# Kernel optimization log

Measured on AMD Instinct MI355X. Metric: run time of the kernel, lower is better.

Reference implementation:

```python
import jax, jax.numpy as jnp
import numpy as np

EPS = 1e-5
K = 20

def lrelu(x):
    return jnp.where(x >= 0, x, 0.2 * x)

def in2d(x):  # [B,C,N,k] instance norm over (N,k), no affine, biased var
    m = jnp.mean(x, axis=(2, 3), keepdims=True)
    v = jnp.var(x, axis=(2, 3), keepdims=True)
    return (x - m) * jax.lax.rsqrt(v + EPS)

def in1d(x):  # [B,C,N] instance norm over N
    m = jnp.mean(x, axis=2, keepdims=True)
    v = jnp.var(x, axis=2, keepdims=True)
    return (x - m) * jax.lax.rsqrt(v + EPS)

def knn_idx(x, k):  # x: [B,C,N]; uses only first 3 channels (as original)
    p = x[:, :3, :]
    inner = -2.0 * jnp.einsum('bcn,bcm->bnm', p, p)
    xx = jnp.sum(p * p, axis=1)  # [B,N]
    pd = -xx[:, :, None] - inner - xx[:, None, :]  # negative squared dist [B,N,N]
    return jax.lax.top_k(pd, k)[1]  # [B,N,k]

def graph_feature(x, k):  # x: [B,C,N] -> [B,2C,N,k]
    idx = knn_idx(x, k)
    xT = jnp.transpose(x, (0, 2, 1))  # [B,N,C]
    feat = jax.vmap(lambda t, i: t[i])(xT, idx)  # [B,N,k,C]
    center = xT[:, :, None, :]
    out = jnp.concatenate([feat - center, jnp.broadcast_to(center, feat.shape)], axis=3)
    return jnp.transpose(out, (0, 3, 1, 2))  # [B,2C,N,k]

def conv2d1(w, x):  # 1x1 conv2d: w [O,C], x [B,C,N,k]
    return jnp.einsum('oc,bcnk->bonk', w, x)

def conv1d1(w, x):  # 1x1 conv1d: w [O,C], x [B,C,N]
    return jnp.einsum('oc,bcn->bon', w, x)

def setup_inputs() -> dict:
    key = jax.random.key(0)
    ks = jax.random.split(key, 10)
    def w(k, o, c):
        return jax.random.normal(k, (o, c), dtype=jnp.float32) * np.float32(1.0 / np.sqrt(c))
    return {
        'x':  jax.random.normal(ks[0], (4, 4096, 4), dtype=jnp.float32),
        'w1': w(ks[1], 64, 8),
        'w2': w(ks[2], 64, 64),
        'w3': w(ks[3], 64, 128),
        'w4': w(ks[4], 64, 64),
        'w5': w(ks[5], 64, 128),
        'w6': w(ks[6], 1024, 192),
        'w7': w(ks[7], 512, 1216),
        'w8': w(ks[8], 256, 512),
        'w9': w(ks[9], 2, 256),
    }

def reference(x, w1, w2, w3, w4, w5, w6, w7, w8, w9):
    xt = jnp.transpose(x, (0, 2, 1))  # [B,4,N]
    num_points = xt.shape[2]
    # EdgeConv block 1
    f = graph_feature(xt, K)                     # [B,8,N,k]
    h = lrelu(in2d(conv2d1(w1, f)))
    h = lrelu(in2d(conv2d1(w2, h)))
    x1 = jnp.max(h, axis=-1)                     # [B,64,N]
    # EdgeConv block 2
    f = graph_feature(x1, K)                     # [B,128,N,k]
    h = lrelu(in2d(conv2d1(w3, f)))
    h = lrelu(in2d(conv2d1(w4, h)))
    x2 = jnp.max(h, axis=-1)
    # EdgeConv block 3
    f = graph_feature(x2, K)
    h = lrelu(in2d(conv2d1(w5, f)))
    x3 = jnp.max(h, axis=-1)
    # global embedding
    cat = jnp.concatenate([x1, x2, x3], axis=1)  # [B,192,N]
    g = lrelu(in1d(conv1d1(w6, cat)))            # [B,1024,N]
    g = jnp.max(g, axis=-1, keepdims=True)       # [B,1024,1]
    g = jnp.broadcast_to(g, (g.shape[0], g.shape[1], num_points))
    h = jnp.concatenate([g, x1, x2, x3], axis=1) # [B,1216,N]
    h = lrelu(in1d(conv1d1(w7, h)))
    h = lrelu(in1d(conv1d1(w8, h)))
    # dropout identity (eval mode)
    out = conv1d1(w9, h)                         # [B,2,N]
    return jnp.transpose(out, (0, 2, 1))         # [B,N,2]
```

## Files before the change

kernel.cpp:

```cpp
#include <hip/hip_runtime.h>
#include <math.h>

constexpr int BB  = 4;
constexpr int NN  = 4096;
constexpr int KK  = 20;
constexpr int NKK = NN * KK;
constexpr int TPOS = BB * NKK;
constexpr int NMASK = NN - 1;

#define DEVFN __device__ __forceinline__

DEVFN float lrelu_f(float v) { return v >= 0.f ? v : 0.2f * v; }
DEVFN unsigned fenc(float f) { unsigned u = __float_as_uint(f); return (u & 0x80000000u) ? ~u : (u | 0x80000000u); }
DEVFN float fdec(unsigned k) { unsigned u = (k & 0x80000000u) ? (k & 0x7fffffffu) : ~k; return __uint_as_float(u); }

template<int CSTRIDE>
__global__ __launch_bounds__(256) void knn_kernel(const float* __restrict__ xin, int* __restrict__ idxout)
{
    __shared__ float sx[NN], sy[NN], sz[NN];
    __shared__ unsigned sdist[NN];
    __shared__ unsigned shist[256];
    __shared__ unsigned scollv[256];
    __shared__ unsigned long long scoll64[128];
    __shared__ unsigned sres[2];
    __shared__ unsigned scnt[2];
    const int tid = threadIdx.x;
    const int b  = blockIdx.x >> 8;
    const int q0 = (blockIdx.x & 255) * 16;
    for (int i = tid; i < NN; i += 256) {
        const float4 rc = *reinterpret_cast<const float4*>(xin + (size_t)(b*NN + i) * CSTRIDE);
        sx[i] = rc.x; sy[i] = rc.y; sz[i] = rc.z;
    }

    for (int qq = 0; qq < 16; ++qq) {
        __syncthreads();
        shist[tid] = 0;
        if (tid == 0) { scnt[0] = 0; scnt[1] = 0; }
        const int qi = q0 + qq;
        const float qx = sx[qi], qy = sy[qi], qz = sz[qi];
        const float nxx = -__fadd_rn(__fadd_rn(__fmul_rn(qx,qx), __fmul_rn(qy,qy)), __fmul_rn(qz,qz));
        __syncthreads();
#pragma unroll
        for (int i = 0; i < NN/256; ++i) {
            const int m = tid + (i << 8);
            float cx = sx[m], cy = sy[m], cz = sz[m];
            float cw  = __fadd_rn(__fadd_rn(__fmul_rn(cx,cx), __fmul_rn(cy,cy)), __fmul_rn(cz,cz));
            float dot = __fadd_rn(__fadd_rn(__fmul_rn(qx,cx), __fmul_rn(qy,cy)), __fmul_rn(qz,cz));
            float pd  = __fsub_rn(__fsub_rn(nxx, __fmul_rn(-2.f, dot)), cw);
            unsigned u = fenc(pd);
            sdist[m] = u;
            atomicAdd(&shist[u >> 24], 1u);
        }
        __syncthreads();
        if (tid < 64) {
            const int base = 255 - tid*4;
            unsigned h0 = shist[base], h1 = shist[base-1], h2 = shist[base-2], h3 = shist[base-3];
            unsigned s = h0 + h1 + h2 + h3;
            unsigned c = s;
#pragma unroll
            for (int off = 1; off < 64; off <<= 1) { unsigned t = __shfl_up(c, off, 64); if (tid >= off) c += t; }
            unsigned cprev = c - s;
            if (c >= KK && cprev < KK) {
                unsigned cc = cprev; int bb = base;
                if (cc + h0 < KK) { cc += h0; bb = base-1;
                    if (cc + h1 < KK) { cc += h1; bb = base-2;
                        if (cc + h2 < KK) { cc += h2; bb = base-3; } } }
                sres[0] = (unsigned)bb; sres[1] = KK - cc;
            }
        }
        __syncthreads();
        const unsigned b0 = sres[0], K1 = sres[1];
        shist[tid] = 0;
        __syncthreads();
#pragma unroll
        for (int i = 0; i < NN/256; ++i) {
            unsigned u = sdist[tid + (i << 8)];
            if ((u >> 24) == b0) atomicAdd(&shist[(u >> 16) & 255u], 1u);
        }
        __syncthreads();
        if (tid < 64) {
            const int base = 255 - tid*4;
            unsigned h0 = shist[base], h1 = shist[base-1], h2 = shist[base-2], h3 = shist[base-3];
            unsigned s = h0 + h1 + h2 + h3;
            unsigned c = s;
#pragma unroll
            for (int off = 1; off < 64; off <<= 1) { unsigned t = __shfl_up(c, off, 64); if (tid >= off) c += t; }
            unsigned cprev = c - s;
            if (c >= K1 && cprev < K1) {
                unsigned cc = cprev; int bb = base;
                if (cc + h0 < K1) { cc += h0; bb = base-1;
                    if (cc + h1 < K1) { cc += h1; bb = base-2;
                        if (cc + h2 < K1) { cc += h2; bb = base-3; } } }
                sres[0] = (unsigned)bb; sres[1] = K1 - cc;
            }
        }
        __syncthreads();
        const unsigned prefix16 = (b0 << 8) | sres[0];
        const unsigned K2 = sres[1];
#pragma unroll
        for (int i = 0; i < NN/256; ++i) {
            unsigned u = sdist[tid + (i << 8)];
            if ((u >> 16) == prefix16) {
                unsigned pos = atomicAdd(&scnt[0], 1u);
                if (pos < 256u) scollv[pos] = u;
            }
        }
        __syncthreads();
        {
            int cb = (int)scnt[0]; if (cb > 256) cb = 256;
            if (tid < cb) {
                unsigned v = scollv[tid];
                unsigned ng = 0, ne = 0;
                for (int j = 0; j < cb; ++j) {
                    unsigned w = scollv[j];
                    ng += (w > v); ne += (w == v);
                }
                if (ng < K2 && ng + ne >= K2) sres[0] = v;
            }
        }
        __syncthreads();
        const unsigned W = sres[0];
#pragma unroll
        for (int i = 0; i < NN/256; ++i) {
            const int m = tid + (i << 8);
            unsigned u = sdist[m];
            if (u >= W) {
                unsigned pos = atomicAdd(&scnt[1], 1u);
                if (pos < 128u) scoll64[pos] = ((unsigned long long)u << 32) | (unsigned)(NN-1 - m);
            }
        }
        __syncthreads();
        {
            int c2 = (int)scnt[1]; if (c2 > 128) c2 = 128;
            if (tid < c2) {
                unsigned long long kv = scoll64[tid];
                int rank = 0;
                for (int j = 0; j < c2; ++j) rank += (scoll64[j] > kv);
                if (rank < KK) {
                    int* op = idxout + ((size_t)(b*NN + qi)) * KK;
                    op[rank] = (NN-1) - (int)(kv & 0xFFFFFFFFull);
                }
            }
        }
    }
}

template<int CINH, int CSTRIDE>
__global__ __launch_bounds__(64) void uv_kernel(const float* __restrict__ xin, const float* __restrict__ w,
                                                float* __restrict__ ub, float* __restrict__ vb)
{
    __shared__ float sp[32][CINH];
    const int lane = threadIdx.x;
    float wa[CINH], wd[CINH];
#pragma unroll
    for (int c = 0; c < CINH; ++c) {
        float a = w[lane*(2*CINH) + c];
        wa[c] = a;
        wd[c] = w[lane*(2*CINH) + CINH + c] - a;
    }
    const int p0 = blockIdx.x * 32;
    for (int i = lane; i < 32*CINH; i += 64) {
        int pi = i / CINH, c = i % CINH;
        sp[pi][c] = xin[(size_t)(p0 + pi)*CSTRIDE + c];
    }
    __syncthreads();
    for (int pi = 0; pi < 32; ++pi) {
        float au = 0.f, av = 0.f;
#pragma unroll
        for (int c = 0; c < CINH; ++c) {
            float xv = sp[pi][c];
            au = fmaf(wa[c], xv, au);
            av = fmaf(wd[c], xv, av);
        }
        ub[(size_t)(p0 + pi)*64 + lane] = au;
        vb[(size_t)(p0 + pi)*64 + lane] = av;
    }
}

template<bool STOREMAX>
__global__ __launch_bounds__(64) void gstat_kernel(const float* __restrict__ ub, const float* __restrict__ vb,
    const int* __restrict__ idx, float* __restrict__ xraw,
    double* __restrict__ ssum, double* __restrict__ ssq)
{
    const int lane = threadIdx.x;
    const int g0 = blockIdx.x * 8;
    const int b = g0 / NN;
    double lsum = 0.0, lsq = 0.0;
    for (int ni = 0; ni < 8; ++ni) {
        const int g = g0 + ni;
        const float v = vb[(size_t)g*64 + lane];
        float vmax = -INFINITY;
        for (int k = 0; k < KK; ++k) {
            const int j = idx[(size_t)g*KK + k] & NMASK;
            float o = ub[(size_t)(b*NN + j)*64 + lane] + v;
            if constexpr (STOREMAX) vmax = fmaxf(vmax, o);
            lsum += (double)o; lsq += (double)o*(double)o;
        }
        if constexpr (STOREMAX) xraw[(size_t)g*64 + lane] = vmax;
    }
    atomicAdd(&ssum[b*64+lane], lsum);
    atomicAdd(&ssq [b*64+lane], lsq);
}

__global__ __launch_bounds__(64) void s1b_kernel(const float* __restrict__ x, const int* __restrict__ idx,
    const float* __restrict__ w1, const float* __restrict__ w2,
    const float* __restrict__ m1, const float* __restrict__ r1,
    float* __restrict__ xraw, double* __restrict__ ssum, double* __restrict__ ssq)
{
    __shared__ float sh[64];
    const int lane = threadIdx.x;
    float wr1[8];
#pragma unroll
    for (int c = 0; c < 8; ++c) wr1[c] = w1[lane*8 + c];
    float wr2[64];
#pragma unroll
    for (int c = 0; c < 64; ++c) wr2[c] = w2[lane*64 + c];
    const int g0 = blockIdx.x * 8;
    const int b = g0 / NN;
    const float mm = m1[b*64+lane], rr = r1[b*64+lane];
    double lsum = 0.0, lsq = 0.0;
    for (int ni = 0; ni < 8; ++ni) {
        const int g = g0 + ni;
        const float4 ct = *reinterpret_cast<const float4*>(x + (size_t)g*4);
        float vmax = -INFINITY;
        for (int k = 0; k < KK; ++k) {
            const int j = idx[(size_t)g*KK + k] & NMASK;
            const float4 nb = *reinterpret_cast<const float4*>(x + (size_t)(b*NN + j)*4);
            float o1 = wr1[0]*(nb.x-ct.x) + wr1[1]*(nb.y-ct.y) + wr1[2]*(nb.z-ct.z) + wr1[3]*(nb.w-ct.w)
                     + wr1[4]*ct.x + wr1[5]*ct.y + wr1[6]*ct.z + wr1[7]*ct.w;
            float h = lrelu_f((o1 - mm) * rr);
            __syncthreads();
            sh[lane] = h;
            __syncthreads();
            float acc = 0.f;
#pragma unroll
            for (int c = 0; c < 64; c += 4) {
                const float4 hv = *reinterpret_cast<const float4*>(&sh[c]);
                acc += wr2[c]*hv.x + wr2[c+1]*hv.y + wr2[c+2]*hv.z + wr2[c+3]*hv.w;
            }
            vmax = fmaxf(vmax, acc);
            lsum += (double)acc; lsq += (double)acc*(double)acc;
        }
        xraw[(size_t)g*64 + lane] = vmax;
    }
    atomicAdd(&ssum[b*64+lane], lsum);
    atomicAdd(&ssq [b*64+lane], lsq);
}

__global__ __launch_bounds__(64) void s2b_kernel(const float* __restrict__ xin, const int* __restrict__ idx,
    const float* __restrict__ w3, const float* __restrict__ w4,
    const float* __restrict__ m3, const float* __restrict__ r3,
    float* __restrict__ xraw, double* __restrict__ ssum, double* __restrict__ ssq)
{
    __shared__ float sf[128];
    __shared__ float sh[64];
    const int lane = threadIdx.x;
    float wr3[128];
#pragma unroll
    for (int c = 0; c < 128; ++c) wr3[c] = w3[lane*128 + c];
    float wr4[64];
#pragma unroll
    for (int c = 0; c < 64; ++c) wr4[c] = w4[lane*64 + c];
    const int g0 = blockIdx.x * 8;
    const int b = g0 / NN;
    const float mm = m3[b*64+lane], rr = r3[b*64+lane];
    double lsum = 0.0, lsq = 0.0;
    for (int ni = 0; ni < 8; ++ni) {
        const int g = g0 + ni;
        const float ctl = xin[(size_t)g*64 + lane];
        float vmax = -INFINITY;
        for (int k = 0; k < KK; ++k) {
            const int j = idx[(size_t)g*KK + k] & NMASK;
            const float nbl = xin[(size_t)(b*NN + j)*64 + lane];
            __syncthreads();
            sf[lane] = nbl - ctl;
            sf[64+lane] = ctl;
            __syncthreads();
            float o3 = 0.f;
#pragma unroll
            for (int c = 0; c < 128; c += 4) {
                const float4 fv = *reinterpret_cast<const float4*>(&sf[c]);
                o3 += wr3[c]*fv.x + wr3[c+1]*fv.y + wr3[c+2]*fv.z + wr3[c+3]*fv.w;
            }
            float h = lrelu_f((o3 - mm) * rr);
            __syncthreads();
            sh[lane] = h;
            __syncthreads();
            float acc = 0.f;
#pragma unroll
            for (int c = 0; c < 64; c += 4) {
                const float4 hv = *reinterpret_cast<const float4*>(&sh[c]);
                acc += wr4[c]*hv.x + wr4[c+1]*hv.y + wr4[c+2]*hv.z + wr4[c+3]*hv.w;
            }
            vmax = fmaxf(vmax, acc);
            lsum += (double)acc; lsq += (double)acc*(double)acc;
        }
        xraw[(size_t)g*64 + lane] = vmax;
    }
    atomicAdd(&ssum[b*64+lane], lsum);
    atomicAdd(&ssq [b*64+lane], lsq);
}

__global__ void fin_kernel(const double* __restrict__ ssum, const double* __restrict__ ssq,
                           float* __restrict__ meanp, float* __restrict__ rstdp, int total, double invn)
{
    int t = blockIdx.x*256 + threadIdx.x;
    if (t >= total) return;
    double m = ssum[t]*invn;
    double v = ssq[t]*invn - m*m;
    meanp[t] = (float)m;
    rstdp[t] = (float)(1.0 / sqrt(v + 1e-5));
}

__global__ void finx_kernel(float* __restrict__ xv, const float* __restrict__ m, const float* __restrict__ r)
{
    int t = blockIdx.x*256 + threadIdx.x;
    int c0 = (t & 15) * 4;
    int b = t >> 16;
    float4 v = *reinterpret_cast<float4*>(xv + (size_t)t*4);
    v.x = lrelu_f((v.x - m[b*64+c0+0]) * r[b*64+c0+0]);
    v.y = lrelu_f((v.y - m[b*64+c0+1]) * r[b*64+c0+1]);
    v.z = lrelu_f((v.z - m[b*64+c0+2]) * r[b*64+c0+2]);
    v.w = lrelu_f((v.w - m[b*64+c0+3]) * r[b*64+c0+3]);
    *reinterpret_cast<float4*>(xv + (size_t)t*4) = v;
}

__global__ void transw_kernel(const float* __restrict__ w, float* __restrict__ wT, int O, int C, int rs, int off)
{
    int t = blockIdx.x*256 + threadIdx.x;
    if (t >= O*C) return;
    int o = t % O, c = t / O;
    wT[t] = w[(size_t)o*rs + off + c];
}

__global__ __launch_bounds__(256) void conv6_kernel(
    const float* __restrict__ x1, const float* __restrict__ x2, const float* __restrict__ x3,
    const float* __restrict__ wT, double* __restrict__ s6sum, double* __restrict__ s6sq, unsigned* __restrict__ s6max)
{
    __shared__ float si[32][192];
    const int b = blockIdx.z, nbase = blockIdx.x*32;
    const int o = blockIdx.y*256 + threadIdx.x;
    for (int i = threadIdx.x; i < 32*192; i += 256) {
        int nl = i/192, c = i%192;
        size_t base = (size_t)(b*NN + nbase + nl)*64;
        si[nl][c] = (c < 64) ? x1[base + c] : (c < 128) ? x2[base + c - 64] : x3[base + c - 128];
    }
    __syncthreads();
    float acc[32];
#pragma unroll
    for (int n = 0; n < 32; ++n) acc[n] = 0.f;
    for (int c = 0; c < 192; ++c) {
        float wv = wT[(size_t)c*1024 + o];
#pragma unroll
        for (int n = 0; n < 32; ++n) acc[n] = fmaf(wv, si[n][c], acc[n]);
    }
    double ps = 0.0, pq = 0.0; float pm = -INFINITY;
#pragma unroll
    for (int n = 0; n < 32; ++n) { ps += (double)acc[n]; pq += (double)acc[n]*(double)acc[n]; pm = fmaxf(pm, acc[n]); }
    atomicAdd(&s6sum[b*1024+o], ps);
    atomicAdd(&s6sq [b*1024+o], pq);
    atomicMax(&s6max[b*1024+o], fenc(pm));
}

__global__ void gfin_kernel(const double* __restrict__ s6sum, const double* __restrict__ s6sq,
                            const unsigned* __restrict__ s6max, float* __restrict__ g)
{
    int t = blockIdx.x*256 + threadIdx.x;
    double m = s6sum[t] * (1.0/4096.0);
    double v = s6sq[t] * (1.0/4096.0) - m*m;
    float rs = (float)(1.0 / sqrt(v + 1e-5));
    g[t] = lrelu_f((fdec(s6max[t]) - (float)m) * rs);
}

__global__ __launch_bounds__(256) void gbias_kernel(const float* __restrict__ w7, const float* __restrict__ g,
                                                    float* __restrict__ gbias)
{
    const int b = blockIdx.y;
    const int o = blockIdx.x*256 + threadIdx.x;
    const float* wr = w7 + (size_t)o*1216;
    const float* gv = g + b*1024;
    float acc = 0.f;
    for (int c = 0; c < 1024; c += 4) {
        float4 wv = *reinterpret_cast<const float4*>(&wr[c]);
        float4 gg = *reinterpret_cast<const float4*>(&gv[c]);
        acc = fmaf(wv.x, gg.x, fmaf(wv.y, gg.y, fmaf(wv.z, gg.z, fmaf(wv.w, gg.w, acc))));
    }
    gbias[b*512+o] = acc;
}

__global__ __launch_bounds__(256) void conv7a_kernel(
    const float* __restrict__ x1, const float* __restrict__ x2, const float* __restrict__ x3,
    const float* __restrict__ wT, const float* __restrict__ gbias,
    double* __restrict__ ssum, double* __restrict__ ssq)
{
    __shared__ float si[32][192];
    const int b = blockIdx.z, nbase = blockIdx.x*32;
    const int o = blockIdx.y*256 + threadIdx.x;
    for (int i = threadIdx.x; i < 32*192; i += 256) {
        int nl = i/192, c = i%192;
        size_t base = (size_t)(b*NN + nbase + nl)*64;
        si[nl][c] = (c < 64) ? x1[base + c] : (c < 128) ? x2[base + c - 64] : x3[base + c - 128];
    }
    __syncthreads();
    float acc[32];
    const float gb = gbias[b*512 + o];
#pragma unroll
    for (int n = 0; n < 32; ++n) acc[n] = gb;
    for (int c = 0; c < 192; ++c) {
        float wv = wT[(size_t)c*512 + o];
#pragma unroll
        for (int n = 0; n < 32; ++n) acc[n] = fmaf(wv, si[n][c], acc[n]);
    }
    double ps = 0.0, pq = 0.0;
#pragma unroll
    for (int n = 0; n < 32; ++n) { ps += (double)acc[n]; pq += (double)acc[n]*(double)acc[n]; }
    atomicAdd(&ssum[b*512+o], ps);
    atomicAdd(&ssq [b*512+o], pq);
}

__global__ __launch_bounds__(256) void conv78_kernel(
    const float* __restrict__ x1, const float* __restrict__ x2, const float* __restrict__ x3,
    const float* __restrict__ wT7, const float* __restrict__ wT8, const float* __restrict__ gbias,
    const float* __restrict__ m7, const float* __restrict__ r7,
    float* __restrict__ out8, double* __restrict__ ssum, double* __restrict__ ssq)
{
    __shared__ float si[16][192];
    __shared__ float h7[16][512];
    const int b = blockIdx.y, nbase = blockIdx.x*16;
    const int tid = threadIdx.x;
    for (int i = tid; i < 16*192; i += 256) {
        int nl = i/192, c = i%192;
        size_t base = (size_t)(b*NN + nbase + nl)*64;
        si[nl][c] = (c < 64) ? x1[base + c] : (c < 128) ? x2[base + c - 64] : x3[base + c - 128];
    }
    __syncthreads();
#pragma unroll
    for (int oo = 0; oo < 512; oo += 256) {
        const int o = oo + tid;
        const float gb = gbias[b*512+o], mm = m7[b*512+o], rr = r7[b*512+o];
        float acc[16];
#pragma unroll
        for (int n = 0; n < 16; ++n) acc[n] = gb;
        for (int c = 0; c < 192; ++c) {
            float wv = wT7[(size_t)c*512 + o];
#pragma unroll
            for (int n = 0; n < 16; ++n) acc[n] = fmaf(wv, si[n][c], acc[n]);
        }
#pragma unroll
        for (int n = 0; n < 16; ++n) h7[n][o] = lrelu_f((acc[n] - mm) * rr);
    }
    __syncthreads();
    const int o = tid;
    float acc8[16];
#pragma unroll
    for (int n = 0; n < 16; ++n) acc8[n] = 0.f;
    for (int c = 0; c < 512; ++c) {
        float wv = wT8[(size_t)c*256 + o];
#pragma unroll
        for (int n = 0; n < 16; ++n) acc8[n] = fmaf(wv, h7[n][c], acc8[n]);
    }
    double ps = 0.0, pq = 0.0;
#pragma unroll
    for (int n = 0; n < 16; ++n) {
        out8[(size_t)(b*NN + nbase + n)*256 + o] = acc8[n];
        ps += (double)acc8[n]; pq += (double)acc8[n]*(double)acc8[n];
    }
    atomicAdd(&ssum[b*256+o], ps);
    atomicAdd(&ssq [b*256+o], pq);
}

__global__ __launch_bounds__(256) void conv9_kernel(const float* __restrict__ in8,
    const float* __restrict__ meanp, const float* __restrict__ rstdp,
    const float* __restrict__ w9, float* __restrict__ outp)
{
    const int lane = threadIdx.x & 63, wv = threadIdx.x >> 6;
    const int ng = blockIdx.x*4 + wv;
    const int b = ng / NN;
    const int c0 = lane*4;
    const float4 v4 = *reinterpret_cast<const float4*>(&in8[(size_t)ng*256 + c0]);
    float vv[4] = {v4.x, v4.y, v4.z, v4.w};
    float a0 = 0.f, a1 = 0.f;
#pragma unroll
    for (int i = 0; i < 4; ++i) {
        int c = c0 + i;
        float a = lrelu_f((vv[i] - meanp[b*256+c]) * rstdp[b*256+c]);
        a0 = fmaf(w9[c],     a, a0);
        a1 = fmaf(w9[256+c], a, a1);
    }
#pragma unroll
    for (int off = 32; off > 0; off >>= 1) {
        a0 += __shfl_down(a0, off, 64);
        a1 += __shfl_down(a1, off, 64);
    }
    if (lane == 0) { outp[(size_t)ng*2 + 0] = a0; outp[(size_t)ng*2 + 1] = a1; }
}

extern "C" void kernel_launch(void* const* d_in, const int* in_sizes, int n_in,
                              void* d_out, int out_size, void* d_ws, size_t ws_size,
                              hipStream_t stream)
{
    const float* x  = (const float*)d_in[0];
    const float* w1 = (const float*)d_in[1];
    const float* w2 = (const float*)d_in[2];
    const float* w3 = (const float*)d_in[3];
    const float* w4 = (const float*)d_in[4];
    const float* w5 = (const float*)d_in[5];
    const float* w6 = (const float*)d_in[6];
    const float* w7 = (const float*)d_in[7];
    const float* w8 = (const float*)d_in[8];
    const float* w9 = (const float*)d_in[9];
    float* outp = (float*)d_out;

    char* ws = (char*)d_ws;
    size_t off = 0;
    auto alloc = [&](size_t bytes) -> void* {
        void* p = ws + off;
        off = (off + bytes + 255) & ~(size_t)255;
        return p;
    };
    double* dstats = (double*)alloc((size_t)16896 * 8);
    unsigned* u6max = (unsigned*)alloc((size_t)4096 * 4);
    float* fstats = (float*)alloc((size_t)14848 * 4);
    int*   idxb  = (int*)  alloc((size_t)TPOS * 4);
    float* wT6   = (float*)alloc((size_t)1024*192*4);
    float* wT7   = (float*)alloc((size_t)512*192*4);
    float* wT8   = (float*)alloc((size_t)256*512*4);
    float* ubuf  = (float*)alloc((size_t)BB*NN*64*4);
    float* vbuf  = (float*)alloc((size_t)BB*NN*64*4);
    float* x1v   = (float*)alloc((size_t)BB*NN*64*4);
    float* x2v   = (float*)alloc((size_t)BB*NN*64*4);
    float* x3v   = (float*)alloc((size_t)BB*NN*64*4);
    float* out8  = (float*)alloc((size_t)BB*NN*256*4);

    double* d1 = dstats;           double* d2 = dstats + 512;
    double* d3 = dstats + 1024;    double* d4 = dstats + 1536;
    double* d5 = dstats + 2048;
    double* d6sum = dstats + 2560; double* d6sq = d6sum + 4096;
    double* d7sum = dstats + 10752; double* d7sq = d7sum + 2048;
    double* d8sum = dstats + 14848; double* d8sq = d8sum + 1024;
    float* m1 = fstats;        float* r1 = fstats + 256;
    float* m2 = fstats + 512;  float* r2 = fstats + 768;
    float* m3 = fstats + 1024; float* r3 = fstats + 1280;
    float* m4 = fstats + 1536; float* r4 = fstats + 1792;
    float* m5 = fstats + 2048; float* r5 = fstats + 2304;
    float* g  = fstats + 2560;
    float* m7 = fstats + 6656; float* r7 = fstats + 8704;
    float* gbias = fstats + 10752;
    float* m8 = fstats + 12800; float* r8 = fstats + 13824;

    hipMemsetAsync(dstats, 0, (size_t)16896*8 + (size_t)4096*4, stream);

    transw_kernel<<<768, 256, 0, stream>>>(w6, wT6, 1024, 192, 192, 0);
    transw_kernel<<<384, 256, 0, stream>>>(w7, wT7, 512, 192, 1216, 1024);
    transw_kernel<<<512, 256, 0, stream>>>(w8, wT8, 256, 512, 512, 0);

    knn_kernel<4><<<1024, 256, 0, stream>>>(x, idxb);
    uv_kernel<4, 4><<<512, 64, 0, stream>>>(x, w1, ubuf, vbuf);
    gstat_kernel<false><<<2048, 64, 0, stream>>>(ubuf, vbuf, idxb, nullptr, d1, d1+256);
    fin_kernel<<<1, 256, 0, stream>>>(d1, d1+256, m1, r1, 256, 1.0/81920.0);
    s1b_kernel<<<2048, 64, 0, stream>>>(x, idxb, w1, w2, m1, r1, x1v, d2, d2+256);
    fin_kernel<<<1, 256, 0, stream>>>(d2, d2+256, m2, r2, 256, 1.0/81920.0);
    finx_kernel<<<1024, 256, 0, stream>>>(x1v, m2, r2);

    knn_kernel<64><<<1024, 256, 0, stream>>>(x1v, idxb);
    uv_kernel<64, 64><<<512, 64, 0, stream>>>(x1v, w3, ubuf, vbuf);
    gstat_kernel<false><<<2048, 64, 0, stream>>>(ubuf, vbuf, idxb, nullptr, d3, d3+256);
    fin_kernel<<<1, 256, 0, stream>>>(d3, d3+256, m3, r3, 256, 1.0/81920.0);
    s2b_kernel<<<2048, 64, 0, stream>>>(x1v, idxb, w3, w4, m3, r3, x2v, d4, d4+256);
    fin_kernel<<<1, 256, 0, stream>>>(d4, d4+256, m4, r4, 256, 1.0/81920.0);
    finx_kernel<<<1024, 256, 0, stream>>>(x2v, m4, r4);

    knn_kernel<64><<<1024, 256, 0, stream>>>(x2v, idxb);
    uv_kernel<64, 64><<<512, 64, 0, stream>>>(x2v, w5, ubuf, vbuf);
    gstat_kernel<true><<<2048, 64, 0, stream>>>(ubuf, vbuf, idxb, x3v, d5, d5+256);
    fin_kernel<<<1, 256, 0, stream>>>(d5, d5+256, m5, r5, 256, 1.0/81920.0);
    finx_kernel<<<1024, 256, 0, stream>>>(x3v, m5, r5);

    conv6_kernel<<<dim3(128, 4, 4), 256, 0, stream>>>(x1v, x2v, x3v, wT6, d6sum, d6sq, u6max);
    gfin_kernel<<<16, 256, 0, stream>>>(d6sum, d6sq, u6max, g);
    gbias_kernel<<<dim3(2, 4), 256, 0, stream>>>(w7, g, gbias);

    conv7a_kernel<<<dim3(128, 2, 4), 256, 0, stream>>>(x1v, x2v, x3v, wT7, gbias, d7sum, d7sq);
    fin_kernel<<<8, 256, 0, stream>>>(d7sum, d7sq, m7, r7, 2048, 1.0/4096.0);
    conv78_kernel<<<dim3(256, 4), 256, 0, stream>>>(x1v, x2v, x3v, wT7, wT8, gbias, m7, r7, out8, d8sum, d8sq);
    fin_kernel<<<4, 256, 0, stream>>>(d8sum, d8sq, m8, r8, 1024, 1.0/4096.0);
    conv9_kernel<<<4096, 256, 0, stream>>>(out8, m8, r8, w9, outp);
}
```

Measured before the change: 1.920 ms.

## Store conv7 output in fp16 instead of recomputing it in conv8 kernel

The conv7 stats pass now writes its pre-norm output to an fp16 buffer, and the conv8 kernel reads that buffer and applies instance norm plus leaky ReLU instead of redoing the 192-channel conv7 matmul. The buffer shares workspace memory with the u/v scratch buffers. This removes a duplicated 512x192 GEMM per point at the cost of a 16 MB fp16 write and read. Rounding conv7 activations to half precision adds some numerical error.

New measurement: 1.855 ms. -3.3%, faster.

```diff
diff --git a/kernel.cpp b/kernel.cpp
--- a/kernel.cpp
+++ b/kernel.cpp
@@ -1,4 +1,5 @@
 #include <hip/hip_runtime.h>
+#include <hip/hip_fp16.h>
 #include <math.h>
 
 constexpr int BB  = 4;
@@ -391,7 +392,7 @@
 __global__ __launch_bounds__(256) void conv7a_kernel(
     const float* __restrict__ x1, const float* __restrict__ x2, const float* __restrict__ x3,
     const float* __restrict__ wT, const float* __restrict__ gbias,
-    double* __restrict__ ssum, double* __restrict__ ssq)
+    __half* __restrict__ out7h, double* __restrict__ ssum, double* __restrict__ ssq)
 {
     __shared__ float si[32][192];
     const int b = blockIdx.z, nbase = blockIdx.x*32;
@@ -413,41 +414,26 @@
     }
     double ps = 0.0, pq = 0.0;
 #pragma unroll
-    for (int n = 0; n < 32; ++n) { ps += (double)acc[n]; pq += (double)acc[n]*(double)acc[n]; }
+    for (int n = 0; n < 32; ++n) {
+        out7h[(size_t)(b*NN + nbase + n)*512 + o] = __float2half(acc[n]);
+        ps += (double)acc[n]; pq += (double)acc[n]*(double)acc[n];
+    }
     atomicAdd(&ssum[b*512+o], ps);
     atomicAdd(&ssq [b*512+o], pq);
 }
 
-__global__ __launch_bounds__(256) void conv78_kernel(
-    const float* __restrict__ x1, const float* __restrict__ x2, const float* __restrict__ x3,
-    const float* __restrict__ wT7, const float* __restrict__ wT8, const float* __restrict__ gbias,
-    const float* __restrict__ m7, const float* __restrict__ r7,
+__global__ __launch_bounds__(256) void conv8k_kernel(
+    const __half* __restrict__ out7h, const float* __restrict__ m7, const float* __restrict__ r7,
+    const float* __restrict__ wT8,
     float* __restrict__ out8, double* __restrict__ ssum, double* __restrict__ ssq)
 {
-    __shared__ float si[16][192];
     __shared__ float h7[16][512];
     const int b = blockIdx.y, nbase = blockIdx.x*16;
     const int tid = threadIdx.x;
-    for (int i = tid; i < 16*192; i += 256) {
-        int nl = i/192, c = i%192;
-        size_t base = (size_t)(b*NN + nbase + nl)*64;
-        si[nl][c] = (c < 64) ? x1[base + c] : (c < 128) ? x2[base + c - 64] : x3[base + c - 128];
-    }
-    __syncthreads();
-#pragma unroll
-    for (int oo = 0; oo < 512; oo += 256) {
-        const int o = oo + tid;
-        const float gb = gbias[b*512+o], mm = m7[b*512+o], rr = r7[b*512+o];
-        float acc[16];
-#pragma unroll
-        for (int n = 0; n < 16; ++n) acc[n] = gb;
-        for (int c = 0; c < 192; ++c) {
-            float wv = wT7[(size_t)c*512 + o];
-#pragma unroll
-            for (int n = 0; n < 16; ++n) acc[n] = fmaf(wv, si[n][c], acc[n]);
-        }
-#pragma unroll
-        for (int n = 0; n < 16; ++n) h7[n][o] = lrelu_f((acc[n] - mm) * rr);
+    for (int i = tid; i < 16*512; i += 256) {
+        int nl = i >> 9, c = i & 511;
+        float v = __half2float(out7h[(size_t)(b*NN + nbase + nl)*512 + c]);
+        h7[nl][c] = lrelu_f((v - m7[b*512+c]) * r7[b*512+c]);
     }
     __syncthreads();
     const int o = tid;
@@ -525,8 +511,10 @@
     float* wT6   = (float*)alloc((size_t)1024*192*4);
     float* wT7   = (float*)alloc((size_t)512*192*4);
     float* wT8   = (float*)alloc((size_t)256*512*4);
-    float* ubuf  = (float*)alloc((size_t)BB*NN*64*4);
-    float* vbuf  = (float*)alloc((size_t)BB*NN*64*4);
+    char*  sc17  = (char*) alloc((size_t)BB*NN*512*2);
+    float* ubuf  = (float*)sc17;
+    float* vbuf  = (float*)(sc17 + (size_t)BB*NN*64*4);
+    __half* out7h = (__half*)sc17;
     float* x1v   = (float*)alloc((size_t)BB*NN*64*4);
     float* x2v   = (float*)alloc((size_t)BB*NN*64*4);
     float* x3v   = (float*)alloc((size_t)BB*NN*64*4);
@@ -580,9 +568,9 @@
     gfin_kernel<<<16, 256, 0, stream>>>(d6sum, d6sq, u6max, g);
     gbias_kernel<<<dim3(2, 4), 256, 0, stream>>>(w7, g, gbias);
 
-    conv7a_kernel<<<dim3(128, 2, 4), 256, 0, stream>>>(x1v, x2v, x3v, wT7, gbias, d7sum, d7sq);
+    conv7a_kernel<<<dim3(128, 2, 4), 256, 0, stream>>>(x1v, x2v, x3v, wT7, gbias, out7h, d7sum, d7sq);
     fin_kernel<<<8, 256, 0, stream>>>(d7sum, d7sq, m7, r7, 2048, 1.0/4096.0);
-    conv78_kernel<<<dim3(256, 4), 256, 0, stream>>>(x1v, x2v, x3v, wT7, wT8, gbias, m7, r7, out8, d8sum, d8sq);
+    conv8k_kernel<<<dim3(256, 4), 256, 0, stream>>>(out7h, m7, r7, wT8, out8, d8sum, d8sq);
     fin_kernel<<<4, 256, 0, stream>>>(d8sum, d8sq, m8, r8, 1024, 1.0/4096.0);
     conv9_kernel<<<4096, 256, 0, stream>>>(out8, m8, r8, w9, outp);
 }
```
